# Kernel optimization log

Hardware: AMD Instinct MI355X
Metric: run time of the kernel (lower is better)

The kernel has to match this reference:

```python
import jax, jax.numpy as jnp
import numpy as np

L = 96
K = 3  # conv kernel size

def setup_inputs() -> dict:
    key = jax.random.key(0)
    ks = jax.random.split(key, 6)
    linear_x = jax.random.randint(ks[0], (4 * L**3,), 0, 2, dtype=jnp.int32)
    tetraeder_2 = jax.random.normal(ks[1], (2, 2), dtype=jnp.float32)
    w1 = jax.random.normal(ks[2], (K, K, K, 12, 16), dtype=jnp.float32) * 0.05
    b1 = jnp.zeros((16,), dtype=jnp.float32)
    w2 = jax.random.normal(ks[3], (K, K, K, 16, 32), dtype=jnp.float32) * 0.05
    b2 = jnp.zeros((32,), dtype=jnp.float32)
    wd = jax.random.normal(ks[4], (32, 1), dtype=jnp.float32) * 0.1
    return {"linear_x": linear_x, "tetraeder_2": tetraeder_2,
            "w1": w1, "b1": b1, "w2": w2, "b2": b2, "wd": wd}

def _bonds(linear_x, tetraeder_2):
    # x: (L,L,L,4) spin config; v: (L,L,L,4,d) per-site vectors via gather
    x = linear_x.reshape(L, L, L, 4)
    v = tetraeder_2[x]
    v0, v1, v2, v3 = v[..., 0, :], v[..., 1, :], v[..., 2, :], v[..., 3, :]
    # roll(v, 1, ax)[a] == v[(a-1) % L] -> periodic neighbor cells cell_1/2/3
    r1 = jnp.roll(v1, 1, axis=0)
    r2 = jnp.roll(v2, 1, axis=1)
    r3 = jnp.roll(v3, 1, axis=2)
    dot = lambda a, b: jnp.einsum('...d,...d->...', a, b)
    # 12 bonds in the exact order of on_unit_cell
    bonds = [dot(v0, v1), dot(v0, v2), dot(v0, v3),
             dot(v0, r1), dot(v0, r2), dot(v0, r3),
             dot(v1, v2), dot(v2, v3), dot(v3, v1),
             dot(r1, r2), dot(r2, r3), dot(r3, r1)]
    return jnp.stack(bonds, axis=-1)  # (L,L,L,12)

def _conv_block(y, w, b):
    pad = [(0, 0)] + [((K - 1) // 2, K // 2)] * 3 + [(0, 0)]
    y = jnp.pad(y, pad, mode='wrap')
    y = jax.lax.conv_general_dilated(
        y, w, window_strides=(1, 1, 1), padding='VALID',
        dimension_numbers=('NDHWC', 'DHWIO', 'NDHWC'))
    return jax.nn.elu(y + b)

def reference(linear_x, tetraeder_2, w1, b1, w2, b2, wd):
    y = _bonds(linear_x, tetraeder_2)[jnp.newaxis, ...]  # (1,L,L,L,12)
    y = _conv_block(y, w1, b1)
    y = _conv_block(y, w2, b2)
    y = jnp.mean(y, axis=(1, 2, 3)).ravel()  # (32,)
    return (y @ wd).ravel()[0]
```

## Files before the change

### kernel.cpp

```cpp
#include <hip/hip_runtime.h>
#include <hip/hip_bf16.h>
#include <cmath>

#define L 96
#define L3 (L*L*L)
#define NCONV 3456

#define BSTRIDE 456

__device__ __constant__ const int TAU[27] = {
    0,16,32, 288,304,320, 576,592,608,
    1728,1744,1760, 2016,2032,2048, 2304,2320,2336,
    3456,3472,3488, 3744,3760,3776, 4032,4048,4064};

typedef __attribute__((ext_vector_type(8))) short short8;
typedef __attribute__((ext_vector_type(4))) float floatx4;

__device__ __forceinline__ float eluf(float x) {
    float e = __expf(x) - 1.0f;
    return x > 0.0f ? x : e;
}

__device__ __forceinline__ unsigned short f2bf(float f) {
    __hip_bfloat16 h = __float2bfloat16(f);
    return *reinterpret_cast<unsigned short*>(&h);
}

__device__ __forceinline__ int wrapc(int x) {
    if (x < 0) x += L;
    if (x >= L) x -= L;
    return x;
}

__global__ __launch_bounds__(256) void prep_kernel(
    const int* __restrict__ lx, const float* __restrict__ tet,
    const float* __restrict__ w1, const float* __restrict__ w2,
    unsigned short* __restrict__ bnd,
    unsigned short* __restrict__ Bm1, unsigned short* __restrict__ Bm2)
{
    int idx = blockIdx.x * 256 + threadIdx.x;

    if (idx < 16*BSTRIDE) {
        int o = idx / BSTRIDE, k = idx % BSTRIDE;
        int tau = k >> 4, i = k & 15;
        float v = (k < 448 && tau < 27 && i < 12) ? w1[tau*192 + i*16 + o] : 0.0f;
        Bm1[idx] = f2bf(v);
    }
    int j = idx - 16*BSTRIDE;
    if (j >= 0 && j < 32*BSTRIDE) {
        int o = j / BSTRIDE, k = j % BSTRIDE;
        int tau = k >> 4;
        int i = k & 15;
        float v = (k < 448 && tau < 27) ? w2[tau*512 + i*32 + o] : 0.0f;
        Bm2[j] = f2bf(v);
    }

    int w = idx % L;
    int t = idx / L;
    int h = t % L;
    int d = t / L;

    float t00 = tet[0], t01 = tet[1], t10 = tet[2], t11 = tet[3];
    float d00 = t00*t00 + t01*t01;
    float d01 = t00*t10 + t01*t11;
    float d11 = t10*t10 + t11*t11;

    const int4 sv = *reinterpret_cast<const int4*>(lx + 4*idx);
    int s0 = sv.x, s1 = sv.y, s2 = sv.z, s3 = sv.w;
    int dm = (d == 0) ? L-1 : d-1;
    int hm = (h == 0) ? L-1 : h-1;
    int wm = (w == 0) ? L-1 : w-1;
    int r1 = lx[4*((dm*L + h)*L + w) + 1];
    int r2 = lx[4*((d*L + hm)*L + w) + 2];
    int r3 = lx[4*((d*L + h)*L + wm) + 3];

    auto dot = [&](int a, int b) -> float {
        return (a == b) ? (a ? d11 : d00) : d01;
    };

    union { unsigned short s[16]; int4 q[2]; } u;
    u.s[0]  = f2bf(dot(s0, s1));
    u.s[1]  = f2bf(dot(s0, s2));
    u.s[2]  = f2bf(dot(s0, s3));
    u.s[3]  = f2bf(dot(s0, r1));
    u.s[4]  = f2bf(dot(s0, r2));
    u.s[5]  = f2bf(dot(s0, r3));
    u.s[6]  = f2bf(dot(s1, s2));
    u.s[7]  = f2bf(dot(s2, s3));
    u.s[8]  = f2bf(dot(s3, s1));
    u.s[9]  = f2bf(dot(r1, r2));
    u.s[10] = f2bf(dot(r2, r3));
    u.s[11] = f2bf(dot(r3, r1));
    u.s[12] = 0; u.s[13] = 0; u.s[14] = 0; u.s[15] = 0;

    int4* dst = reinterpret_cast<int4*>(bnd + (size_t)idx*16);
    dst[0] = u.q[0];
    dst[1] = u.q[1];
}

__device__ __forceinline__ void stage_tile(
    const unsigned short* __restrict__ x, unsigned short* __restrict__ tile,
    int W0, int H0, int D0, int tid)
{
    #pragma unroll
    for (int i = 0; i < 6; ++i) {
        int t = tid + i*256;
        if (i < 5 || t < 1296) {
            int row = t / 36, off = t - row*36;
            int dd = row / 6, hh = row - dd*6;
            int gd = wrapc(D0 + dd - 1);
            int gh = wrapc(H0 + hh - 1);
            int vox = off >> 1, half = off & 1;
            int gw = wrapc(W0 + vox - 1);
            size_t gi = ((size_t)((gd*L + gh)*L + gw))*16 + half*8;
            __builtin_amdgcn_global_load_lds(
                (const __attribute__((address_space(1))) unsigned int*)(x + gi),
                (__attribute__((address_space(3))) unsigned int*)(tile + t*8),
                16, 0, 0);
        }
    }
}

__device__ __forceinline__ void stage_bmat(
    const unsigned short* __restrict__ Bm, unsigned short* __restrict__ Bls,
    int nxfer, int tid)
{
    #pragma unroll
    for (int i = 0; i < 8; ++i) {
        int t = tid + i*256;
        if (t < nxfer) {
            __builtin_amdgcn_global_load_lds(
                (const __attribute__((address_space(1))) unsigned int*)(Bm + t*8),
                (__attribute__((address_space(3))) unsigned int*)(Bls + t*8),
                16, 0, 0);
        }
    }
}

__global__ __launch_bounds__(256, 4) void conv1_kernel(
    const unsigned short* __restrict__ x, const unsigned short* __restrict__ Bm,
    const float* __restrict__ bias, unsigned short* __restrict__ y)
{
    __shared__ __attribute__((aligned(16))) unsigned short tile[6*6*18*16];
    __shared__ __attribute__((aligned(16))) unsigned short Bls[16*BSTRIDE];
    int tid = threadIdx.x;
    int W0 = blockIdx.x * 16, H0 = blockIdx.y * 4, D0 = blockIdx.z * 4;

    stage_tile(x, tile, W0, H0, D0, tid);
    stage_bmat(Bm, Bls, 912, tid);
    __syncthreads();

    int lane = tid & 63, wave = tid >> 6;
    int laneV = lane & 15, g = lane >> 4;
    int gb = g >> 1;
    int abase = laneV*16 + (g & 1)*8;

    floatx4 acc[4];
    #pragma unroll
    for (int m = 0; m < 4; ++m) acc[m] = (floatx4)(0.0f);

    int moff[4];
    #pragma unroll
    for (int m = 0; m < 4; ++m) {
        int mt = wave*4 + m;
        moff[m] = (((mt >> 2)*6 + (mt & 3))*18)*16;
    }

    short8 aC[4], aN[4], bC, bN;
    {
        int a0 = abase + (gb ? TAU[1] : TAU[0]);
        bC = *reinterpret_cast<const short8*>(&Bls[laneV*BSTRIDE + g*8]);
        #pragma unroll
        for (int m = 0; m < 4; ++m)
            aC[m] = *reinterpret_cast<const short8*>(&tile[moff[m] + a0]);
    }

    #pragma unroll
    for (int kt = 0; kt < 14; ++kt) {
        if (kt < 13) {
            int tev = TAU[2*(kt+1)];
            int tod = TAU[(2*(kt+1)+1 > 26) ? 26 : 2*(kt+1)+1];
            int an = abase + (gb ? tod : tev);
            bN = *reinterpret_cast<const short8*>(&Bls[laneV*BSTRIDE + (kt+1)*32 + g*8]);
            #pragma unroll
            for (int m = 0; m < 4; ++m)
                aN[m] = *reinterpret_cast<const short8*>(&tile[moff[m] + an]);
        }
        #pragma unroll
        for (int m = 0; m < 4; ++m)
            acc[m] = __builtin_amdgcn_mfma_f32_16x16x32_bf16(aC[m], bC, acc[m], 0, 0, 0);
        if (kt < 13) {
            #pragma unroll
            for (int m = 0; m < 4; ++m) aC[m] = aN[m];
            bC = bN;
        }
    }

    float bch = bias[laneV];
    #pragma unroll
    for (int m = 0; m < 4; ++m) {
        int mt = wave*4 + m;
        int d = D0 + (mt >> 2), h = H0 + (mt & 3);
        int wb = W0 + g*4;
        size_t base = ((size_t)((d*L + h)*L + wb))*16 + laneV;
        #pragma unroll
        for (int reg = 0; reg < 4; ++reg) {
            y[base + (size_t)reg*16] = f2bf(eluf(acc[m][reg] + bch));
        }
    }
}

__global__ __launch_bounds__(256, 4) void conv2_kernel(
    const unsigned short* __restrict__ x, const unsigned short* __restrict__ Bm,
    const float* __restrict__ bias, const float* __restrict__ wd,
    float* __restrict__ partials)
{
    __shared__ __attribute__((aligned(16))) unsigned short tile[6*6*18*16];
    __shared__ __attribute__((aligned(16))) unsigned short Bls[32*BSTRIDE];
    __shared__ float red[4];
    int tid = threadIdx.x;
    int W0 = blockIdx.x * 16, H0 = blockIdx.y * 4, D0 = blockIdx.z * 4;

    stage_tile(x, tile, W0, H0, D0, tid);
    stage_bmat(Bm, Bls, 1824, tid);
    __syncthreads();

    int lane = tid & 63, wave = tid >> 6;
    int laneV = lane & 15, g = lane >> 4;
    int gb = g >> 1;
    int abase = laneV*16 + (g & 1)*8;

    floatx4 acc[4][2];
    #pragma unroll
    for (int m = 0; m < 4; ++m) {
        acc[m][0] = (floatx4)(0.0f);
        acc[m][1] = (floatx4)(0.0f);
    }

    int moff[4];
    #pragma unroll
    for (int m = 0; m < 4; ++m) {
        int mt = wave*4 + m;
        moff[m] = (((mt >> 2)*6 + (mt & 3))*18)*16;
    }

    short8 aC[4], aN[4], bC0, bC1, bN0, bN1;
    {
        int a0 = abase + (gb ? TAU[1] : TAU[0]);
        bC0 = *reinterpret_cast<const short8*>(&Bls[laneV*BSTRIDE + g*8]);
        bC1 = *reinterpret_cast<const short8*>(&Bls[(16 + laneV)*BSTRIDE + g*8]);
        #pragma unroll
        for (int m = 0; m < 4; ++m)
            aC[m] = *reinterpret_cast<const short8*>(&tile[moff[m] + a0]);
    }

    #pragma unroll
    for (int kt = 0; kt < 14; ++kt) {
        if (kt < 13) {
            int tev = TAU[2*(kt+1)];
            int tod = TAU[(2*(kt+1)+1 > 26) ? 26 : 2*(kt+1)+1];
            int an = abase + (gb ? tod : tev);
            bN0 = *reinterpret_cast<const short8*>(&Bls[laneV*BSTRIDE + (kt+1)*32 + g*8]);
            bN1 = *reinterpret_cast<const short8*>(&Bls[(16 + laneV)*BSTRIDE + (kt+1)*32 + g*8]);
            #pragma unroll
            for (int m = 0; m < 4; ++m)
                aN[m] = *reinterpret_cast<const short8*>(&tile[moff[m] + an]);
        }
        #pragma unroll
        for (int m = 0; m < 4; ++m) {
            acc[m][0] = __builtin_amdgcn_mfma_f32_16x16x32_bf16(aC[m], bC0, acc[m][0], 0, 0, 0);
            acc[m][1] = __builtin_amdgcn_mfma_f32_16x16x32_bf16(aC[m], bC1, acc[m][1], 0, 0, 0);
        }
        if (kt < 13) {
            #pragma unroll
            for (int m = 0; m < 4; ++m) aC[m] = aN[m];
            bC0 = bN0; bC1 = bN1;
        }
    }

    float b2a = bias[laneV], b2b = bias[16 + laneV];
    float wda = wd[laneV],  wdb = wd[16 + laneV];
    float s = 0.0f;
    #pragma unroll
    for (int m = 0; m < 4; ++m) {
        #pragma unroll
        for (int reg = 0; reg < 4; ++reg) {
            s += eluf(acc[m][0][reg] + b2a) * wda;
            s += eluf(acc[m][1][reg] + b2b) * wdb;
        }
    }

    #pragma unroll
    for (int off = 32; off; off >>= 1) s += __shfl_down(s, off);
    if (lane == 0) red[wave] = s;
    __syncthreads();
    if (tid == 0) {
        int bid = (blockIdx.z * gridDim.y + blockIdx.y) * gridDim.x + blockIdx.x;
        partials[bid] = red[0] + red[1] + red[2] + red[3];
    }
}

__global__ __launch_bounds__(256) void final_kernel(
    const float* __restrict__ partials, float* __restrict__ out)
{
    float s = 0.0f;
    for (int i = threadIdx.x; i < NCONV; i += 256) s += partials[i];
    #pragma unroll
    for (int off = 32; off; off >>= 1) s += __shfl_down(s, off);
    __shared__ float red[4];
    int lane = threadIdx.x & 63;
    int wv   = threadIdx.x >> 6;
    if (lane == 0) red[wv] = s;
    __syncthreads();
    if (threadIdx.x == 0)
        out[0] = (red[0] + red[1] + red[2] + red[3]) * (1.0f / (float)L3);
}

extern "C" void kernel_launch(void* const* d_in, const int* in_sizes, int n_in,
                              void* d_out, int out_size, void* d_ws, size_t ws_size,
                              hipStream_t stream) {
    const int*   lx  = (const int*)  d_in[0];
    const float* tet = (const float*)d_in[1];
    const float* w1  = (const float*)d_in[2];
    const float* b1  = (const float*)d_in[3];
    const float* w2  = (const float*)d_in[4];
    const float* b2  = (const float*)d_in[5];
    const float* wd  = (const float*)d_in[6];
    float* out = (float*)d_out;

    char* ws = (char*)d_ws;
    const size_t ARR_BYTES = (size_t)L3 * 16 * 2;
    unsigned short* bnd  = (unsigned short*)ws;
    unsigned short* y1   = (unsigned short*)(ws + ARR_BYTES);
    unsigned short* Bm1  = (unsigned short*)(ws + 2*ARR_BYTES);
    unsigned short* Bm2  = (unsigned short*)(ws + 2*ARR_BYTES + 16*BSTRIDE*2);
    float* partials      = (float*)         (ws + 2*ARR_BYTES + 48*BSTRIDE*2);

    prep_kernel<<<L3/256, 256, 0, stream>>>(lx, tet, w1, w2, bnd, Bm1, Bm2);
    conv1_kernel<<<dim3(6,24,24), 256, 0, stream>>>(bnd, Bm1, b1, y1);
    conv2_kernel<<<dim3(6,24,24), 256, 0, stream>>>(y1, Bm2, b2, wd, partials);
    final_kernel<<<1, 256, 0, stream>>>(partials, out);
}
```

Measured before the change: 148.9 us.

## Make conv blocks persistent over depth with double-buffered tile staging

Each conv block now processes four consecutive depth slabs instead of one, so there are a quarter as many blocks. The weight matrix is staged into LDS once per block rather than once per slab. The next input tile is staged asynchronously into a second LDS buffer while the current one is computed. The change also remaps block IDs with an XCD-style swizzle and raises MFMA issue priority with s_setprio. In exchange, LDS use doubles and launch bounds drop to 2 blocks per CU, giving fewer resident waves and a smaller grid (864 blocks) that may leave CUs underused.

```diff
diff --git a/kernel.cpp b/kernel.cpp
--- a/kernel.cpp
+++ b/kernel.cpp
@@ -4,8 +4,8 @@
 
 #define L 96
 #define L3 (L*L*L)
-#define NCONV 3456
-
+#define NT 4
+#define NCONV 864
 #define BSTRIDE 456
 
 __device__ __constant__ const int TAU[27] = {
@@ -137,27 +137,35 @@
     }
 }
 
-__global__ __launch_bounds__(256, 4) void conv1_kernel(
+__device__ __forceinline__ void tile_coords(int& bid, int& W0, int& H0, int& Dz)
+{
+    bid = (blockIdx.z * 24 + blockIdx.y) * 6 + blockIdx.x;
+    int nb = (bid & 7) * 108 + (bid >> 3);
+    W0 = (nb % 6) * 16;
+    int t1 = nb / 6;
+    H0 = (t1 % 24) * 4;
+    Dz = t1 / 24;
+}
+
+__global__ __launch_bounds__(256, 2) void conv1_kernel(
     const unsigned short* __restrict__ x, const unsigned short* __restrict__ Bm,
     const float* __restrict__ bias, unsigned short* __restrict__ y)
 {
-    __shared__ __attribute__((aligned(16))) unsigned short tile[6*6*18*16];
+    __shared__ __attribute__((aligned(16))) unsigned short tile[2][6*6*18*16];
     __shared__ __attribute__((aligned(16))) unsigned short Bls[16*BSTRIDE];
     int tid = threadIdx.x;
-    int W0 = blockIdx.x * 16, H0 = blockIdx.y * 4, D0 = blockIdx.z * 4;
-
-    stage_tile(x, tile, W0, H0, D0, tid);
+    int bid, W0, H0, Dz;
+    tile_coords(bid, W0, H0, Dz);
+
     stage_bmat(Bm, Bls, 912, tid);
+    stage_tile(x, tile[0], W0, H0, Dz*16, tid);
     __syncthreads();
 
     int lane = tid & 63, wave = tid >> 6;
     int laneV = lane & 15, g = lane >> 4;
     int gb = g >> 1;
     int abase = laneV*16 + (g & 1)*8;
-
-    floatx4 acc[4];
-    #pragma unroll
-    for (int m = 0; m < 4; ++m) acc[m] = (floatx4)(0.0f);
+    float bch = bias[laneV];
 
     int moff[4];
     #pragma unroll
@@ -166,76 +174,86 @@
         moff[m] = (((mt >> 2)*6 + (mt & 3))*18)*16;
     }
 
-    short8 aC[4], aN[4], bC, bN;
-    {
-        int a0 = abase + (gb ? TAU[1] : TAU[0]);
-        bC = *reinterpret_cast<const short8*>(&Bls[laneV*BSTRIDE + g*8]);
-        #pragma unroll
-        for (int m = 0; m < 4; ++m)
-            aC[m] = *reinterpret_cast<const short8*>(&tile[moff[m] + a0]);
-    }
-
-    #pragma unroll
-    for (int kt = 0; kt < 14; ++kt) {
-        if (kt < 13) {
-            int tev = TAU[2*(kt+1)];
-            int tod = TAU[(2*(kt+1)+1 > 26) ? 26 : 2*(kt+1)+1];
-            int an = abase + (gb ? tod : tev);
-            bN = *reinterpret_cast<const short8*>(&Bls[laneV*BSTRIDE + (kt+1)*32 + g*8]);
+    for (int t = 0; t < NT; ++t) {
+        if (t < NT-1)
+            stage_tile(x, tile[(t+1) & 1], W0, H0, Dz*16 + 4*(t+1), tid);
+
+        const unsigned short* tl = tile[t & 1];
+
+        floatx4 acc[4];
+        #pragma unroll
+        for (int m = 0; m < 4; ++m) acc[m] = (floatx4)(0.0f);
+
+        short8 aC[4], aN[4], bC, bN;
+        {
+            int a0 = abase + (gb ? TAU[1] : TAU[0]);
+            bC = *reinterpret_cast<const short8*>(&Bls[laneV*BSTRIDE + g*8]);
             #pragma unroll
             for (int m = 0; m < 4; ++m)
-                aN[m] = *reinterpret_cast<const short8*>(&tile[moff[m] + an]);
-        }
-        #pragma unroll
-        for (int m = 0; m < 4; ++m)
-            acc[m] = __builtin_amdgcn_mfma_f32_16x16x32_bf16(aC[m], bC, acc[m], 0, 0, 0);
-        if (kt < 13) {
-            #pragma unroll
-            for (int m = 0; m < 4; ++m) aC[m] = aN[m];
-            bC = bN;
-        }
-    }
-
-    float bch = bias[laneV];
-    #pragma unroll
-    for (int m = 0; m < 4; ++m) {
-        int mt = wave*4 + m;
-        int d = D0 + (mt >> 2), h = H0 + (mt & 3);
-        int wb = W0 + g*4;
-        size_t base = ((size_t)((d*L + h)*L + wb))*16 + laneV;
-        #pragma unroll
-        for (int reg = 0; reg < 4; ++reg) {
-            y[base + (size_t)reg*16] = f2bf(eluf(acc[m][reg] + bch));
-        }
-    }
-}
-
-__global__ __launch_bounds__(256, 4) void conv2_kernel(
+                aC[m] = *reinterpret_cast<const short8*>(&tl[moff[m] + a0]);
+        }
+
+        #pragma unroll
+        for (int kt = 0; kt < 14; ++kt) {
+            if (kt < 13) {
+                int tev = TAU[2*(kt+1)];
+                int tod = TAU[(2*(kt+1)+1 > 26) ? 26 : 2*(kt+1)+1];
+                int an = abase + (gb ? tod : tev);
+                bN = *reinterpret_cast<const short8*>(&Bls[laneV*BSTRIDE + (kt+1)*32 + g*8]);
+                #pragma unroll
+                for (int m = 0; m < 4; ++m)
+                    aN[m] = *reinterpret_cast<const short8*>(&tl[moff[m] + an]);
+            }
+            __builtin_amdgcn_s_setprio(1);
+            #pragma unroll
+            for (int m = 0; m < 4; ++m)
+                acc[m] = __builtin_amdgcn_mfma_f32_16x16x32_bf16(aC[m], bC, acc[m], 0, 0, 0);
+            __builtin_amdgcn_s_setprio(0);
+            if (kt < 13) {
+                #pragma unroll
+                for (int m = 0; m < 4; ++m) aC[m] = aN[m];
+                bC = bN;
+            }
+        }
+
+        int D0 = Dz*16 + t*4;
+        #pragma unroll
+        for (int m = 0; m < 4; ++m) {
+            int mt = wave*4 + m;
+            int d = D0 + (mt >> 2), h = H0 + (mt & 3);
+            int wb = W0 + g*4;
+            size_t base = ((size_t)((d*L + h)*L + wb))*16 + laneV;
+            #pragma unroll
+            for (int reg = 0; reg < 4; ++reg) {
+                y[base + (size_t)reg*16] = f2bf(eluf(acc[m][reg] + bch));
+            }
+        }
+        __syncthreads();
+    }
+}
+
+__global__ __launch_bounds__(256, 2) void conv2_kernel(
     const unsigned short* __restrict__ x, const unsigned short* __restrict__ Bm,
     const float* __restrict__ bias, const float* __restrict__ wd,
     float* __restrict__ partials)
 {
-    __shared__ __attribute__((aligned(16))) unsigned short tile[6*6*18*16];
+    __shared__ __attribute__((aligned(16))) unsigned short tile[2][6*6*18*16];
     __shared__ __attribute__((aligned(16))) unsigned short Bls[32*BSTRIDE];
     __shared__ float red[4];
     int tid = threadIdx.x;
-    int W0 = blockIdx.x * 16, H0 = blockIdx.y * 4, D0 = blockIdx.z * 4;
-
-    stage_tile(x, tile, W0, H0, D0, tid);
+    int bid, W0, H0, Dz;
+    tile_coords(bid, W0, H0, Dz);
+
     stage_bmat(Bm, Bls, 1824, tid);
+    stage_tile(x, tile[0], W0, H0, Dz*16, tid);
     __syncthreads();
 
     int lane = tid & 63, wave = tid >> 6;
     int laneV = lane & 15, g = lane >> 4;
     int gb = g >> 1;
     int abase = laneV*16 + (g & 1)*8;
-
-    floatx4 acc[4][2];
-    #pragma unroll
-    for (int m = 0; m < 4; ++m) {
-        acc[m][0] = (floatx4)(0.0f);
-        acc[m][1] = (floatx4)(0.0f);
-    }
+    float b2a = bias[laneV], b2b = bias[16 + laneV];
+    float wda = wd[laneV],  wdb = wd[16 + laneV];
 
     int moff[4];
     #pragma unroll
@@ -244,50 +262,66 @@
         moff[m] = (((mt >> 2)*6 + (mt & 3))*18)*16;
     }
 
-    short8 aC[4], aN[4], bC0, bC1, bN0, bN1;
-    {
-        int a0 = abase + (gb ? TAU[1] : TAU[0]);
-        bC0 = *reinterpret_cast<const short8*>(&Bls[laneV*BSTRIDE + g*8]);
-        bC1 = *reinterpret_cast<const short8*>(&Bls[(16 + laneV)*BSTRIDE + g*8]);
-        #pragma unroll
-        for (int m = 0; m < 4; ++m)
-            aC[m] = *reinterpret_cast<const short8*>(&tile[moff[m] + a0]);
-    }
-
-    #pragma unroll
-    for (int kt = 0; kt < 14; ++kt) {
-        if (kt < 13) {
-            int tev = TAU[2*(kt+1)];
-            int tod = TAU[(2*(kt+1)+1 > 26) ? 26 : 2*(kt+1)+1];
-            int an = abase + (gb ? tod : tev);
-            bN0 = *reinterpret_cast<const short8*>(&Bls[laneV*BSTRIDE + (kt+1)*32 + g*8]);
-            bN1 = *reinterpret_cast<const short8*>(&Bls[(16 + laneV)*BSTRIDE + (kt+1)*32 + g*8]);
+    float s = 0.0f;
+
+    for (int t = 0; t < NT; ++t) {
+        if (t < NT-1)
+            stage_tile(x, tile[(t+1) & 1], W0, H0, Dz*16 + 4*(t+1), tid);
+
+        const unsigned short* tl = tile[t & 1];
+
+        floatx4 acc[4][2];
+        #pragma unroll
+        for (int m = 0; m < 4; ++m) {
+            acc[m][0] = (floatx4)(0.0f);
+            acc[m][1] = (floatx4)(0.0f);
+        }
+
+        short8 aC[4], aN[4], bC0, bC1, bN0, bN1;
+        {
+            int a0 = abase + (gb ? TAU[1] : TAU[0]);
+            bC0 = *reinterpret_cast<const short8*>(&Bls[laneV*BSTRIDE + g*8]);
+            bC1 = *reinterpret_cast<const short8*>(&Bls[(16 + laneV)*BSTRIDE + g*8]);
             #pragma unroll
             for (int m = 0; m < 4; ++m)
-                aN[m] = *reinterpret_cast<const short8*>(&tile[moff[m] + an]);
-        }
+                aC[m] = *reinterpret_cast<const short8*>(&tl[moff[m] + a0]);
+        }
+
+        #pragma unroll
+        for (int kt = 0; kt < 14; ++kt) {
+            if (kt < 13) {
+                int tev = TAU[2*(kt+1)];
+                int tod = TAU[(2*(kt+1)+1 > 26) ? 26 : 2*(kt+1)+1];
+                int an = abase + (gb ? tod : tev);
+                bN0 = *reinterpret_cast<const short8*>(&Bls[laneV*BSTRIDE + (kt+1)*32 + g*8]);
+                bN1 = *reinterpret_cast<const short8*>(&Bls[(16 + laneV)*BSTRIDE + (kt+1)*32 + g*8]);
+                #pragma unroll
+                for (int m = 0; m < 4; ++m)
+                    aN[m] = *reinterpret_cast<const short8*>(&tl[moff[m] + an]);
+            }
+            __builtin_amdgcn_s_setprio(1);
+            #pragma unroll
+            for (int m = 0; m < 4; ++m) {
+                acc[m][0] = __builtin_amdgcn_mfma_f32_16x16x32_bf16(aC[m], bC0, acc[m][0], 0, 0, 0);
+                acc[m][1] = __builtin_amdgcn_mfma_f32_16x16x32_bf16(aC[m], bC1, acc[m][1], 0, 0, 0);
+            }
+            __builtin_amdgcn_s_setprio(0);
+            if (kt < 13) {
+                #pragma unroll
+                for (int m = 0; m < 4; ++m) aC[m] = aN[m];
+                bC0 = bN0; bC1 = bN1;
+            }
+        }
+
         #pragma unroll
         for (int m = 0; m < 4; ++m) {
-            acc[m][0] = __builtin_amdgcn_mfma_f32_16x16x32_bf16(aC[m], bC0, acc[m][0], 0, 0, 0);
-            acc[m][1] = __builtin_amdgcn_mfma_f32_16x16x32_bf16(aC[m], bC1, acc[m][1], 0, 0, 0);
-        }
-        if (kt < 13) {
-            #pragma unroll
-            for (int m = 0; m < 4; ++m) aC[m] = aN[m];
-            bC0 = bN0; bC1 = bN1;
-        }
-    }
-
-    float b2a = bias[laneV], b2b = bias[16 + laneV];
-    float wda = wd[laneV],  wdb = wd[16 + laneV];
-    float s = 0.0f;
-    #pragma unroll
-    for (int m = 0; m < 4; ++m) {
-        #pragma unroll
-        for (int reg = 0; reg < 4; ++reg) {
-            s += eluf(acc[m][0][reg] + b2a) * wda;
-            s += eluf(acc[m][1][reg] + b2b) * wdb;
-        }
+            #pragma unroll
+            for (int reg = 0; reg < 4; ++reg) {
+                s += eluf(acc[m][0][reg] + b2a) * wda;
+                s += eluf(acc[m][1][reg] + b2b) * wdb;
+            }
+        }
+        __syncthreads();
     }
 
     #pragma unroll
@@ -295,7 +329,6 @@
     if (lane == 0) red[wave] = s;
     __syncthreads();
     if (tid == 0) {
-        int bid = (blockIdx.z * gridDim.y + blockIdx.y) * gridDim.x + blockIdx.x;
         partials[bid] = red[0] + red[1] + red[2] + red[3];
     }
 }
@@ -337,7 +370,7 @@
     float* partials      = (float*)         (ws + 2*ARR_BYTES + 48*BSTRIDE*2);
 
     prep_kernel<<<L3/256, 256, 0, stream>>>(lx, tet, w1, w2, bnd, Bm1, Bm2);
-    conv1_kernel<<<dim3(6,24,24), 256, 0, stream>>>(bnd, Bm1, b1, y1);
-    conv2_kernel<<<dim3(6,24,24), 256, 0, stream>>>(y1, Bm2, b2, wd, partials);
+    conv1_kernel<<<dim3(6,24,6), 256, 0, stream>>>(bnd, Bm1, b1, y1);
+    conv2_kernel<<<dim3(6,24,6), 256, 0, stream>>>(y1, Bm2, b2, wd, partials);
     final_kernel<<<1, 256, 0, stream>>>(partials, out);
 }
```

New measurement: 151.1 us. About the same (+1.4%).
